# Kernel tuning notes

Hardware: AMD Instinct MI355X
Metric: run time of the kernel (lower is better)

The kernel has to match this reference:

```python
import jax, jax.numpy as jnp
import numpy as np

N_STATE = 1024
N_HEAD = 16
HEAD_DIM = N_STATE // N_HEAD


def setup_inputs() -> dict:
    key = jax.random.key(0)
    ks = jax.random.split(key, 8)
    s = 0.02
    return {
        "x": jax.random.normal(ks[0], (4, 1500, N_STATE), dtype=jnp.float32),
        "Wq": jax.random.normal(ks[1], (N_STATE, N_STATE), dtype=jnp.float32) * s,
        "bq": jnp.zeros((N_STATE,), dtype=jnp.float32),
        "Wk": jax.random.normal(ks[2], (N_STATE, N_STATE), dtype=jnp.float32) * s,
        "Wv": jax.random.normal(ks[3], (N_STATE, N_STATE), dtype=jnp.float32) * s,
        "bv": jnp.zeros((N_STATE,), dtype=jnp.float32),
        "Wo": jax.random.normal(ks[4], (N_STATE, N_STATE), dtype=jnp.float32) * s,
        "bo": jnp.zeros((N_STATE,), dtype=jnp.float32),
    }


def reference(x, Wq, bq, Wk, Wv, bv, Wo, bo):
    B, S, _ = x.shape
    scale = HEAD_DIM ** (-0.5)
    # projections (torch Linear: y = x @ W.T + b)
    q = x @ Wq.T + bq
    k = x @ Wk.T
    v = x @ Wv.T + bv
    # [B, H, S, D]
    q = q.reshape(B, S, N_HEAD, HEAD_DIM).transpose(0, 2, 1, 3)
    k = k.reshape(B, S, N_HEAD, HEAD_DIM).transpose(0, 2, 1, 3)
    v = v.reshape(B, S, N_HEAD, HEAD_DIM).transpose(0, 2, 1, 3)
    # scores scaled AFTER the matmul, as in the original (qk * qk_scale)
    qk = jnp.einsum("bhqd,bhkd->bhqk", q, k) * scale
    w = jax.nn.softmax(qk, axis=-1)
    wv = jnp.einsum("bhqk,bhkd->bhqd", w, v)
    wv = wv.transpose(0, 2, 1, 3).reshape(B, S, N_STATE)
    return wv @ Wo.T + bo
```

## Files before the change

kernel.cpp:

```cpp
#include <hip/hip_runtime.h>
#include <stdint.h>

#define S_LEN  1500
#define S_PAD  1536
#define BATCH  4
#define NSTATE 1024
#define NHEAD  16
#define HDIM   64
#define MROWS  6000
#define C1 0.180336879f

typedef __attribute__((ext_vector_type(8)))  short short8;
typedef __attribute__((ext_vector_type(4)))  float floatx4;
typedef __attribute__((ext_vector_type(16))) float floatx16;

__device__ __forceinline__ unsigned short f2bf(float f) {
  union { float f; unsigned int u; } v; v.f = f;
  unsigned int r = v.u + 0x7fffu + ((v.u >> 16) & 1u);
  return (unsigned short)(r >> 16);
}

__device__ __forceinline__ void gld_lds16(const void* g, void* l) {
  __builtin_amdgcn_global_load_lds(
      (const __attribute__((address_space(1))) void*)g,
      (__attribute__((address_space(3))) void*)l, 16, 0, 0);
}

__global__ __launch_bounds__(256) void cvt_all(
    const float* __restrict__ x,  const float* __restrict__ Wq,
    const float* __restrict__ Wk, const float* __restrict__ Wv,
    const float* __restrict__ Wo, unsigned short* __restrict__ dst)
{
  const size_t NX = (size_t)MROWS * NSTATE;
  size_t e = ((size_t)blockIdx.x * 256 + threadIdx.x) * 4;
  const float* src; size_t off;
  if (e < NX) { src = x; off = e; }
  else {
    size_t t = e - NX;
    int wsel = (int)(t >> 20);
    off = t & ((1u << 20) - 1);
    src = (wsel == 0) ? Wq : (wsel == 1) ? Wk : (wsel == 2) ? Wv : Wo;
  }
  float4 v = *(const float4*)(src + off);
  uint2 o;
  o.x = (unsigned int)f2bf(v.x) | ((unsigned int)f2bf(v.y) << 16);
  o.y = (unsigned int)f2bf(v.z) | ((unsigned int)f2bf(v.w) << 16);
  *(uint2*)(dst + e) = o;
}

template <bool F32OUT>
__device__ __forceinline__ void gemm128_bt(
    const unsigned short* __restrict__ X,
    const unsigned short* __restrict__ W,
    const float* __restrict__ bias,
    void* __restrict__ Yv,
    int m0, int n0, float oscale)
{
  __shared__ unsigned short As[2][128 * 32];
  __shared__ unsigned short Bs[2][128 * 32];

  const int tid  = threadIdx.x;
  const int lane = tid & 63;
  const int wid  = tid >> 6;
  const int wm   = (wid & 1) * 64;
  const int wn   = (wid >> 1) * 64;
  const int l15  = lane & 15;
  const int l4   = lane >> 4;

  floatx4 acc[4][4];
#pragma unroll
  for (int i = 0; i < 4; ++i)
#pragma unroll
    for (int j = 0; j < 4; ++j)
      acc[i][j] = (floatx4){0.f, 0.f, 0.f, 0.f};

  const int srow  = tid >> 2;
  const int scolb = (tid & 3) * 16;

  const char* xrp[2];
  const char* wrp[2];
#pragma unroll
  for (int r = 0; r < 2; ++r) {
    int arow = m0 + r * 64 + srow;
    if (arow > MROWS - 1) arow = MROWS - 1;
    xrp[r] = (const char*)X + (size_t)arow * NSTATE * 2 + scolb;
    int brow = n0 + r * 64 + srow;
    wrp[r] = (const char*)W + (size_t)brow * NSTATE * 2 + scolb;
  }

  for (int k0 = 0; k0 < NSTATE; k0 += 64) {
    __syncthreads();
#pragma unroll
    for (int h = 0; h < 2; ++h) {
      int kb = (k0 + h * 32) * 2;
#pragma unroll
      for (int r = 0; r < 2; ++r) {
        gld_lds16(xrp[r] + kb, (char*)As[h] + r * 4096 + wid * 1024);
        gld_lds16(wrp[r] + kb, (char*)Bs[h] + r * 4096 + wid * 1024);
      }
    }
    __syncthreads();

#pragma unroll
    for (int h = 0; h < 2; ++h) {
      short8 a[4], b[4];
#pragma unroll
      for (int i = 0; i < 4; ++i)
        a[i] = *(const short8*)(As[h] + (wm + i * 16 + l15) * 32 + l4 * 8);
#pragma unroll
      for (int j = 0; j < 4; ++j)
        b[j] = *(const short8*)(Bs[h] + (wn + j * 16 + l15) * 32 + l4 * 8);
#pragma unroll
      for (int i = 0; i < 4; ++i)
#pragma unroll
        for (int j = 0; j < 4; ++j)
          acc[i][j] = __builtin_amdgcn_mfma_f32_16x16x32_bf16(a[i], b[j], acc[i][j], 0, 0, 0);
    }
  }

#pragma unroll
  for (int j = 0; j < 4; ++j) {
    int ng = n0 + wn + j * 16 + l15;
    float bias_v = bias ? bias[ng] : 0.f;
#pragma unroll
    for (int i = 0; i < 4; ++i) {
      int mgb = m0 + wm + i * 16 + l4 * 4;
#pragma unroll
      for (int r = 0; r < 4; ++r) {
        int mg = mgb + r;
        if (mg < MROWS) {
          float val = (acc[i][j][r] + bias_v) * oscale;
          if (F32OUT) ((float*)Yv)[(size_t)mg * NSTATE + ng] = val;
          else        ((unsigned short*)Yv)[(size_t)mg * NSTATE + ng] = f2bf(val);
        }
      }
    }
  }
}

__global__ __launch_bounds__(256) void proj_qkv(
    const unsigned short* __restrict__ X,
    const unsigned short* __restrict__ Wq, const unsigned short* __restrict__ Wk,
    const unsigned short* __restrict__ Wv,
    const float* __restrict__ bq, const float* __restrict__ bv,
    unsigned short* __restrict__ q, unsigned short* __restrict__ k,
    unsigned short* __restrict__ v)
{
  const int id  = blockIdx.x;
  const int sid = (id & 7) * 141 + (id >> 3);
  const int z   = sid / 376;
  const int rem = sid - z * 376;
  const int m0  = (rem >> 3) * 128;
  const int n0  = (rem & 7) * 128;

  const unsigned short* W = (z == 0) ? Wq : (z == 1) ? Wk : Wv;
  const float* bias       = (z == 0) ? bq : (z == 1) ? (const float*)nullptr : bv;
  unsigned short* Y       = (z == 0) ? q  : (z == 1) ? k  : v;
  const float osc         = (z == 0) ? C1 : 1.0f;
  gemm128_bt<false>(X, W, bias, Y, m0, n0, osc);
}

__global__ __launch_bounds__(256) void proj_o(
    const unsigned short* __restrict__ X, const unsigned short* __restrict__ W,
    const float* __restrict__ bias, float* __restrict__ Y)
{
  const int id  = blockIdx.x;
  const int sid = (id & 7) * 47 + (id >> 3);
  gemm128_bt<true>(X, W, bias, Y, (sid >> 3) * 128, (sid & 7) * 128, 1.0f);
}

__global__ __launch_bounds__(256) void vtrans(
    const unsigned short* __restrict__ v, unsigned short* __restrict__ vt)
{
  __shared__ unsigned short T[64][72];
  const int tid = threadIdx.x;
  const int st = blockIdx.x * 64, h = blockIdx.y, b = blockIdx.z;
#pragma unroll
  for (int rr = 0; rr < 2; ++rr) {
    int sl = rr * 32 + (tid >> 3);
    int dl = (tid & 7) * 8;
    int s  = st + sl;
    uint4 val = make_uint4(0u, 0u, 0u, 0u);
    if (s < S_LEN)
      val = *(const uint4*)&v[((size_t)b * S_LEN + s) * NSTATE + h * HDIM + dl];
    *(uint4*)&T[sl][dl] = val;
  }
  __syncthreads();
#pragma unroll
  for (int rr = 0; rr < 2; ++rr) {
    int dl = rr * 32 + (tid >> 3);
    int s0 = (tid & 7) * 8;
    unsigned short tmp[8];
#pragma unroll
    for (int j2 = 0; j2 < 8; ++j2) tmp[j2] = T[s0 + j2][dl];
    *(uint4*)&vt[(((size_t)b * NHEAD + h) * HDIM + dl) * S_PAD + st + s0] =
        *(const uint4*)tmp;
  }
}

#define NHALF 24

__global__ __launch_bounds__(256, 4) void attn32t(
    const unsigned short* __restrict__ Q, const unsigned short* __restrict__ K,
    const unsigned short* __restrict__ VT, unsigned short* __restrict__ O)
{
  __shared__ unsigned short SMEM[16384];
  unsigned short* Os = SMEM;

  const int tid  = threadIdx.x;
  const int lane = tid & 63;
  const int w    = tid >> 6;
  const int l31  = lane & 31;
  const int lhi  = lane >> 5;

  const int id  = blockIdx.x;
  const int sid = (id & 7) * 96 + (id >> 3);
  const int qt  = sid % 12;
  const int hb  = sid / 12;
  const int h   = hb & 15;
  const int b   = hb >> 4;

  const size_t base  = ((size_t)b * S_LEN) * NSTATE + h * HDIM;
  const size_t vbase = (((size_t)b * NHEAD + h) * HDIM) * S_PAD;

  const int srow8 = lane >> 3;
  const int sc3   = lane & 7;

  short8 qf[4];
  {
    int qrow = qt * 128 + w * 32 + l31;
    if (qrow > S_LEN - 1) qrow = S_LEN - 1;
    const unsigned short* qp = Q + base + (size_t)qrow * NSTATE;
#pragma unroll
    for (int c = 0; c < 4; ++c)
      qf[c] = *(const short8*)(qp + c * 16 + lhi * 8);
  }

  short8 ones8;
#pragma unroll
  for (int i = 0; i < 8; ++i) ones8[i] = (short)0x3F80;

  floatx16 oacc[2];
  oacc[0] = (floatx16)(0.f);
  oacc[1] = (floatx16)(0.f);
  floatx16 lacc = (floatx16)(0.f);

  auto stage_half = [&](int u, int bi) {
    char* kbase = (char*)SMEM + bi * 8192;
    char* vbase_l = (char*)SMEM + 16384 + bi * 8192;
#pragma unroll
    for (int qq = 0; qq < 2; ++qq) {
      int cg   = w * 2 + qq;
      int row  = cg * 8 + srow8;
      int logc = sc3 ^ (row & 7);
      int s = u * 64 + row; if (s > S_LEN - 1) s = S_LEN - 1;
      gld_lds16(&K[base + (size_t)s * NSTATE + logc * 8], kbase + cg * 1024);
    }
#pragma unroll
    for (int qq = 0; qq < 2; ++qq) {
      int cg   = w * 2 + qq;
      int d    = cg * 8 + srow8;
      int logc = sc3 ^ (d & 7);
      gld_lds16(&VT[vbase + (size_t)d * S_PAD + u * 64 + logc * 8],
                vbase_l + cg * 1024);
    }
  };

  stage_half(0, 0);
  __syncthreads();

  for (int u = 0; u < NHALF; ++u) {
    const int cur = u & 1;
    if (u < NHALF - 1) stage_half(u + 1, cur ^ 1);

    const unsigned short* Ks  = SMEM + cur * 4096;
    const unsigned short* Vts = SMEM + 8192 + cur * 4096;

#pragma unroll
    for (int kvt = 0; kvt < 2; ++kvt) {
      int row = kvt * 32 + l31;
      floatx16 sacc = (floatx16)(0.f);
      __builtin_amdgcn_s_setprio(1);
#pragma unroll
      for (int c = 0; c < 4; ++c) {
        int phys = (c * 2 + lhi) ^ (row & 7);
        short8 ak = *(const short8*)(Ks + row * 64 + phys * 8);
        sacc = __builtin_amdgcn_mfma_f32_32x32x16_bf16(ak, qf[c], sacc, 0, 0, 0);
      }
      __builtin_amdgcn_s_setprio(0);

      if (u == NHALF - 1) {
        if (kvt == 1) {
#pragma unroll
          for (int r = 0; r < 16; ++r) sacc[r] = -3.0e38f;
        } else {
#pragma unroll
          for (int r = 12; r < 16; ++r) sacc[r] = lhi ? -3.0e38f : sacc[r];
        }
      }

      unsigned int pk[8], ex[8];
#pragma unroll
      for (int i = 0; i < 8; ++i) {
        float plo = exp2f(sacc[2 * i]);
        float phi = exp2f(sacc[2 * i + 1]);
        unsigned int rr;
        asm("v_cvt_pk_bf16_f32 %0, %1, %2" : "=v"(rr) : "v"(plo), "v"(phi));
        pk[i] = rr;
      }
#pragma unroll
      for (int i = 0; i < 8; ++i)
        ex[i] = __shfl_xor((unsigned int)pk[i], 32, 64);

      int4 f0i, f1i;
      f0i.x = lhi ? ex[2] : pk[0];
      f0i.y = lhi ? ex[3] : pk[1];
      f0i.z = lhi ? pk[2] : ex[0];
      f0i.w = lhi ? pk[3] : ex[1];
      f1i.x = lhi ? ex[6] : pk[4];
      f1i.y = lhi ? ex[7] : pk[5];
      f1i.z = lhi ? pk[6] : ex[4];
      f1i.w = lhi ? pk[7] : ex[5];
      short8 f0 = *(short8*)&f0i;
      short8 f1 = *(short8*)&f1i;

      __builtin_amdgcn_s_setprio(1);
      lacc = __builtin_amdgcn_mfma_f32_32x32x16_bf16(ones8, f0, lacc, 0, 0, 0);
      lacc = __builtin_amdgcn_mfma_f32_32x32x16_bf16(ones8, f1, lacc, 0, 0, 0);

#pragma unroll
      for (int dt = 0; dt < 2; ++dt) {
        int d = dt * 32 + l31;
        int p0 = ((kvt * 4 + 0) + lhi) ^ (d & 7);
        int p1 = ((kvt * 4 + 2) + lhi) ^ (d & 7);
        short8 av0 = *(const short8*)(Vts + d * 64 + p0 * 8);
        short8 av1 = *(const short8*)(Vts + d * 64 + p1 * 8);
        oacc[dt] = __builtin_amdgcn_mfma_f32_32x32x16_bf16(av0, f0, oacc[dt], 0, 0, 0);
        oacc[dt] = __builtin_amdgcn_mfma_f32_32x32x16_bf16(av1, f1, oacc[dt], 0, 0, 0);
      }
      __builtin_amdgcn_s_setprio(0);
    }

    __syncthreads();
  }

  float inv = 1.f / lacc[0];

  __syncthreads();
#pragma unroll
  for (int dt = 0; dt < 2; ++dt)
#pragma unroll
    for (int g = 0; g < 4; ++g) {
      int d0 = dt * 32 + g * 8 + lhi * 4;
      float v0 = oacc[dt][4 * g + 0] * inv;
      float v1 = oacc[dt][4 * g + 1] * inv;
      float v2 = oacc[dt][4 * g + 2] * inv;
      float v3 = oacc[dt][4 * g + 3] * inv;
      uint2 pk2;
      pk2.x = (unsigned int)f2bf(v0) | ((unsigned int)f2bf(v1) << 16);
      pk2.y = (unsigned int)f2bf(v2) | ((unsigned int)f2bf(v3) << 16);
      *(uint2*)&Os[(w * 32 + l31) * 72 + d0] = pk2;
    }
  __syncthreads();
#pragma unroll
  for (int pass = 0; pass < 4; ++pass) {
    int e = pass * 256 + tid;
    int row = e >> 3, ch = e & 7;
    int s = qt * 128 + row;
    if (s < S_LEN)
      *(uint4*)&O[base + (size_t)s * NSTATE + ch * 8] = *(const uint4*)&Os[row * 72 + ch * 8];
  }
}

extern "C" void kernel_launch(void* const* d_in, const int* in_sizes, int n_in,
                              void* d_out, int out_size, void* d_ws, size_t ws_size,
                              hipStream_t stream) {
  const float* x  = (const float*)d_in[0];
  const float* Wq = (const float*)d_in[1];
  const float* bq = (const float*)d_in[2];
  const float* Wk = (const float*)d_in[3];
  const float* Wv = (const float*)d_in[4];
  const float* bv = (const float*)d_in[5];
  const float* Wo = (const float*)d_in[6];
  const float* bo = (const float*)d_in[7];
  float* out = (float*)d_out;

  const size_t NX = (size_t)MROWS * NSTATE;
  const size_t NW = (size_t)NSTATE * NSTATE;

  unsigned short* xb  = (unsigned short*)d_ws;
  unsigned short* Wqb = xb  + NX;
  unsigned short* Wkb = Wqb + NW;
  unsigned short* Wvb = Wkb + NW;
  unsigned short* Wob = Wvb + NW;
  unsigned short* q   = Wob + NW;
  unsigned short* k   = q + NX;
  unsigned short* v   = k + NX;
  unsigned short* vt  = v + NX;
  unsigned short* wv  = xb;

  dim3 blk(256);
  const size_t n4_total = (NX + 4 * NW) / 4;
  cvt_all<<<dim3((int)(n4_total / 256)), blk, 0, stream>>>(x, Wq, Wk, Wv, Wo, xb);
  proj_qkv<<<dim3(1128), blk, 0, stream>>>(xb, Wqb, Wkb, Wvb, bq, bv, q, k, v);
  vtrans<<<dim3(24, NHEAD, BATCH), blk, 0, stream>>>(v, vt);
  attn32t<<<dim3(768), blk, 0, stream>>>(q, k, vt, wv);
  proj_o<<<dim3(376), blk, 0, stream>>>(wv, Wob, bo, out);
}
```

Measured before the change: 255.9 us.

## Switch projection GEMMs to 256x256 double-buffered swizzled LDS tiles

Replaces the 128x128 single-stage projection GEMM with a 256x256 tile computed by 512 threads (8 waves, each owning 128x64). The next K-slab is prefetched into a second LDS buffer while the current one is consumed, and the LDS layout is XOR-swizzled to avoid bank conflicts. Wave priority is raised around the MFMA burst. Each tile reuses more data and there is less barrier stalling. The cost is far fewer blocks (288 and 96) on a 256-CU device, about 128KB of LDS per block, and heavy register pressure, which can leave CUs idle and hurt the output projection in particular.

Result: slower. 300.0 us (+17.2%).

```diff
diff --git a/kernel.cpp b/kernel.cpp
--- a/kernel.cpp
+++ b/kernel.cpp
@@ -49,87 +49,106 @@
 }
 
 template <bool F32OUT>
-__device__ __forceinline__ void gemm128_bt(
+__device__ __forceinline__ void gemm256_db(
     const unsigned short* __restrict__ X,
     const unsigned short* __restrict__ W,
     const float* __restrict__ bias,
     void* __restrict__ Yv,
     int m0, int n0, float oscale)
 {
-  __shared__ unsigned short As[2][128 * 32];
-  __shared__ unsigned short Bs[2][128 * 32];
+  __shared__ unsigned short As[2][256 * 64];
+  __shared__ unsigned short Bs[2][256 * 64];
 
   const int tid  = threadIdx.x;
   const int lane = tid & 63;
-  const int wid  = tid >> 6;
-  const int wm   = (wid & 1) * 64;
-  const int wn   = (wid >> 1) * 64;
+  const int w    = tid >> 6;
+  const int wr   = (w >> 2) * 128;
+  const int wc   = (w & 3) * 64;
   const int l15  = lane & 15;
   const int l4   = lane >> 4;
-
-  floatx4 acc[4][4];
-#pragma unroll
-  for (int i = 0; i < 4; ++i)
-#pragma unroll
-    for (int j = 0; j < 4; ++j)
-      acc[i][j] = (floatx4){0.f, 0.f, 0.f, 0.f};
-
-  const int srow  = tid >> 2;
-  const int scolb = (tid & 3) * 16;
-
-  const char* xrp[2];
-  const char* wrp[2];
-#pragma unroll
-  for (int r = 0; r < 2; ++r) {
-    int arow = m0 + r * 64 + srow;
-    if (arow > MROWS - 1) arow = MROWS - 1;
-    xrp[r] = (const char*)X + (size_t)arow * NSTATE * 2 + scolb;
-    int brow = n0 + r * 64 + srow;
-    wrp[r] = (const char*)W + (size_t)brow * NSTATE * 2 + scolb;
-  }
-
-  for (int k0 = 0; k0 < NSTATE; k0 += 64) {
+  const int srow8 = lane >> 3;
+  const int sc    = lane & 7;
+
+  floatx4 acc[8][4];
+#pragma unroll
+  for (int m = 0; m < 8; ++m)
+#pragma unroll
+    for (int n = 0; n < 4; ++n)
+      acc[m][n] = (floatx4){0.f, 0.f, 0.f, 0.f};
+
+  const char* ap[4];
+  const char* bp[4];
+#pragma unroll
+  for (int c = 0; c < 4; ++c) {
+    int r    = c * 64 + w * 8 + srow8;
+    int logc = sc ^ srow8;
+    int gr = m0 + r; if (gr > MROWS - 1) gr = MROWS - 1;
+    ap[c] = (const char*)X + (size_t)gr * NSTATE * 2 + logc * 16;
+    int br = n0 + r;
+    bp[c] = (const char*)W + (size_t)br * NSTATE * 2 + logc * 16;
+  }
+
+  auto stage = [&](int t, int bi) {
+    const int kb = t * 128;
+#pragma unroll
+    for (int c = 0; c < 4; ++c) {
+      gld_lds16(ap[c] + kb, (char*)As[bi] + c * 8192 + w * 1024);
+      gld_lds16(bp[c] + kb, (char*)Bs[bi] + c * 8192 + w * 1024);
+    }
+  };
+
+  stage(0, 0);
+  __syncthreads();
+
+  for (int t = 0; t < 16; ++t) {
+    const int cur = t & 1;
+    if (t < 15) stage(t + 1, cur ^ 1);
+
+    const unsigned short* A = As[cur];
+    const unsigned short* B = Bs[cur];
+
+    short8 bfr[2][4];
+#pragma unroll
+    for (int s = 0; s < 2; ++s)
+#pragma unroll
+      for (int n = 0; n < 4; ++n) {
+        int r    = wc + n * 16 + l15;
+        int phys = (s * 4 + l4) ^ (r & 7);
+        bfr[s][n] = *(const short8*)(B + r * 64 + phys * 8);
+      }
+
+    __builtin_amdgcn_s_setprio(1);
+#pragma unroll
+    for (int m = 0; m < 8; ++m) {
+      int r  = wr + m * 16 + l15;
+      int p0 = (0 + l4) ^ (r & 7);
+      int p1 = (4 + l4) ^ (r & 7);
+      short8 a0 = *(const short8*)(A + r * 64 + p0 * 8);
+      short8 a1 = *(const short8*)(A + r * 64 + p1 * 8);
+#pragma unroll
+      for (int n = 0; n < 4; ++n)
+        acc[m][n] = __builtin_amdgcn_mfma_f32_16x16x32_bf16(a0, bfr[0][n], acc[m][n], 0, 0, 0);
+#pragma unroll
+      for (int n = 0; n < 4; ++n)
+        acc[m][n] = __builtin_amdgcn_mfma_f32_16x16x32_bf16(a1, bfr[1][n], acc[m][n], 0, 0, 0);
+    }
+    __builtin_amdgcn_s_setprio(0);
+
     __syncthreads();
-#pragma unroll
-    for (int h = 0; h < 2; ++h) {
-      int kb = (k0 + h * 32) * 2;
-#pragma unroll
-      for (int r = 0; r < 2; ++r) {
-        gld_lds16(xrp[r] + kb, (char*)As[h] + r * 4096 + wid * 1024);
-        gld_lds16(wrp[r] + kb, (char*)Bs[h] + r * 4096 + wid * 1024);
-      }
-    }
-    __syncthreads();
-
-#pragma unroll
-    for (int h = 0; h < 2; ++h) {
-      short8 a[4], b[4];
-#pragma unroll
-      for (int i = 0; i < 4; ++i)
-        a[i] = *(const short8*)(As[h] + (wm + i * 16 + l15) * 32 + l4 * 8);
-#pragma unroll
-      for (int j = 0; j < 4; ++j)
-        b[j] = *(const short8*)(Bs[h] + (wn + j * 16 + l15) * 32 + l4 * 8);
-#pragma unroll
-      for (int i = 0; i < 4; ++i)
-#pragma unroll
-        for (int j = 0; j < 4; ++j)
-          acc[i][j] = __builtin_amdgcn_mfma_f32_16x16x32_bf16(a[i], b[j], acc[i][j], 0, 0, 0);
-    }
-  }
-
-#pragma unroll
-  for (int j = 0; j < 4; ++j) {
-    int ng = n0 + wn + j * 16 + l15;
+  }
+
+#pragma unroll
+  for (int n = 0; n < 4; ++n) {
+    int ng = n0 + wc + n * 16 + l15;
     float bias_v = bias ? bias[ng] : 0.f;
 #pragma unroll
-    for (int i = 0; i < 4; ++i) {
-      int mgb = m0 + wm + i * 16 + l4 * 4;
-#pragma unroll
-      for (int r = 0; r < 4; ++r) {
-        int mg = mgb + r;
+    for (int m = 0; m < 8; ++m) {
+      int mgb = m0 + wr + m * 16 + l4 * 4;
+#pragma unroll
+      for (int ri = 0; ri < 4; ++ri) {
+        int mg = mgb + ri;
         if (mg < MROWS) {
-          float val = (acc[i][j][r] + bias_v) * oscale;
+          float val = (acc[m][n][ri] + bias_v) * oscale;
           if (F32OUT) ((float*)Yv)[(size_t)mg * NSTATE + ng] = val;
           else        ((unsigned short*)Yv)[(size_t)mg * NSTATE + ng] = f2bf(val);
         }
@@ -138,7 +157,7 @@
   }
 }
 
-__global__ __launch_bounds__(256) void proj_qkv(
+__global__ __launch_bounds__(512, 2) void proj_qkv(
     const unsigned short* __restrict__ X,
     const unsigned short* __restrict__ Wq, const unsigned short* __restrict__ Wk,
     const unsigned short* __restrict__ Wv,
@@ -147,26 +166,26 @@
     unsigned short* __restrict__ v)
 {
   const int id  = blockIdx.x;
-  const int sid = (id & 7) * 141 + (id >> 3);
-  const int z   = sid / 376;
-  const int rem = sid - z * 376;
-  const int m0  = (rem >> 3) * 128;
-  const int n0  = (rem & 7) * 128;
+  const int sid = (id & 7) * 36 + (id >> 3);
+  const int mt  = sid / 12;
+  const int rem = sid % 12;
+  const int z   = rem >> 2;
+  const int n0  = (rem & 3) * 256;
 
   const unsigned short* W = (z == 0) ? Wq : (z == 1) ? Wk : Wv;
   const float* bias       = (z == 0) ? bq : (z == 1) ? (const float*)nullptr : bv;
   unsigned short* Y       = (z == 0) ? q  : (z == 1) ? k  : v;
   const float osc         = (z == 0) ? C1 : 1.0f;
-  gemm128_bt<false>(X, W, bias, Y, m0, n0, osc);
-}
-
-__global__ __launch_bounds__(256) void proj_o(
+  gemm256_db<false>(X, W, bias, Y, mt * 256, n0, osc);
+}
+
+__global__ __launch_bounds__(512, 2) void proj_o(
     const unsigned short* __restrict__ X, const unsigned short* __restrict__ W,
     const float* __restrict__ bias, float* __restrict__ Y)
 {
   const int id  = blockIdx.x;
-  const int sid = (id & 7) * 47 + (id >> 3);
-  gemm128_bt<true>(X, W, bias, Y, (sid >> 3) * 128, (sid & 7) * 128, 1.0f);
+  const int sid = (id & 7) * 12 + (id >> 3);
+  gemm256_db<true>(X, W, bias, Y, (sid >> 2) * 256, (sid & 3) * 256, 1.0f);
 }
 
 __global__ __launch_bounds__(256) void vtrans(
@@ -399,11 +418,10 @@
   unsigned short* vt  = v + NX;
   unsigned short* wv  = xb;
 
-  dim3 blk(256);
   const size_t n4_total = (NX + 4 * NW) / 4;
-  cvt_all<<<dim3((int)(n4_total / 256)), blk, 0, stream>>>(x, Wq, Wk, Wv, Wo, xb);
-  proj_qkv<<<dim3(1128), blk, 0, stream>>>(xb, Wqb, Wkb, Wvb, bq, bv, q, k, v);
-  vtrans<<<dim3(24, NHEAD, BATCH), blk, 0, stream>>>(v, vt);
-  attn32t<<<dim3(768), blk, 0, stream>>>(q, k, vt, wv);
-  proj_o<<<dim3(376), blk, 0, stream>>>(wv, Wob, bo, out);
-}
+  cvt_all<<<dim3((int)(n4_total / 256)), dim3(256), 0, stream>>>(x, Wq, Wk, Wv, Wo, xb);
+  proj_qkv<<<dim3(288), dim3(512), 0, stream>>>(xb, Wqb, Wkb, Wvb, bq, bv, q, k, v);
+  vtrans<<<dim3(24, NHEAD, BATCH), dim3(256), 0, stream>>>(v, vt);
+  attn32t<<<dim3(768), dim3(256), 0, stream>>>(q, k, vt, wv);
+  proj_o<<<dim3(96), dim3(512), 0, stream>>>(wv, Wob, bo, out);
+}
```

## Switch GEMMs to 32x32 MFMA with swizzled LDS and fuse V transpose into projection

Applied to the files above, without the earlier changes.

The shared GEMM now uses 32x32x16 bf16 MFMA tiles with an XOR-swizzled LDS layout in place of 16x16x32 tiles, aiming to cut LDS bank conflicts and instruction count. The V projection epilogue writes straight into the transposed, padded vt layout, which removes the separate vtrans kernel and the round trip through an intermediate v buffer. A memset zeroes the padding of vt on each call. The transposed epilogue issues scattered 8-byte stores with a per-element division to recover the batch index, which may hurt store coalescing.

Result: no change. 256.1 us (+0.1%).

```diff
diff --git a/kernel.cpp b/kernel.cpp
--- a/kernel.cpp
+++ b/kernel.cpp
@@ -48,13 +48,12 @@
   *(uint2*)(dst + e) = o;
 }
 
-template <bool F32OUT>
-__device__ __forceinline__ void gemm128_bt(
+__device__ __forceinline__ void gemm128_32(
     const unsigned short* __restrict__ X,
     const unsigned short* __restrict__ W,
     const float* __restrict__ bias,
     void* __restrict__ Yv,
-    int m0, int n0, float oscale)
+    int m0, int n0, float oscale, int outmode)
 {
   __shared__ unsigned short As[2][128 * 32];
   __shared__ unsigned short Bs[2][128 * 32];
@@ -64,18 +63,19 @@
   const int wid  = tid >> 6;
   const int wm   = (wid & 1) * 64;
   const int wn   = (wid >> 1) * 64;
-  const int l15  = lane & 15;
-  const int l4   = lane >> 4;
-
-  floatx4 acc[4][4];
-#pragma unroll
-  for (int i = 0; i < 4; ++i)
-#pragma unroll
-    for (int j = 0; j < 4; ++j)
-      acc[i][j] = (floatx4){0.f, 0.f, 0.f, 0.f};
-
-  const int srow  = tid >> 2;
-  const int scolb = (tid & 3) * 16;
+  const int l31  = lane & 31;
+  const int lhi  = lane >> 5;
+  const int fr   = (l31 >> 1) & 3;
+
+  floatx16 acc[2][2];
+#pragma unroll
+  for (int i = 0; i < 2; ++i)
+#pragma unroll
+    for (int j = 0; j < 2; ++j)
+      acc[i][j] = (floatx16)(0.f);
+
+  const int srow = tid >> 2;
+  const int logc = (lane & 3) ^ ((srow >> 1) & 3);
 
   const char* xrp[2];
   const char* wrp[2];
@@ -83,9 +83,9 @@
   for (int r = 0; r < 2; ++r) {
     int arow = m0 + r * 64 + srow;
     if (arow > MROWS - 1) arow = MROWS - 1;
-    xrp[r] = (const char*)X + (size_t)arow * NSTATE * 2 + scolb;
+    xrp[r] = (const char*)X + (size_t)arow * NSTATE * 2 + logc * 16;
     int brow = n0 + r * 64 + srow;
-    wrp[r] = (const char*)W + (size_t)brow * NSTATE * 2 + scolb;
+    wrp[r] = (const char*)W + (size_t)brow * NSTATE * 2 + logc * 16;
   }
 
   for (int k0 = 0; k0 < NSTATE; k0 += 64) {
@@ -103,37 +103,77 @@
 
 #pragma unroll
     for (int h = 0; h < 2; ++h) {
-      short8 a[4], b[4];
-#pragma unroll
-      for (int i = 0; i < 4; ++i)
-        a[i] = *(const short8*)(As[h] + (wm + i * 16 + l15) * 32 + l4 * 8);
-#pragma unroll
-      for (int j = 0; j < 4; ++j)
-        b[j] = *(const short8*)(Bs[h] + (wn + j * 16 + l15) * 32 + l4 * 8);
-#pragma unroll
-      for (int i = 0; i < 4; ++i)
-#pragma unroll
-        for (int j = 0; j < 4; ++j)
-          acc[i][j] = __builtin_amdgcn_mfma_f32_16x16x32_bf16(a[i], b[j], acc[i][j], 0, 0, 0);
-    }
-  }
-
-#pragma unroll
-  for (int j = 0; j < 4; ++j) {
-    int ng = n0 + wn + j * 16 + l15;
-    float bias_v = bias ? bias[ng] : 0.f;
-#pragma unroll
-    for (int i = 0; i < 4; ++i) {
-      int mgb = m0 + wm + i * 16 + l4 * 4;
-#pragma unroll
-      for (int r = 0; r < 4; ++r) {
-        int mg = mgb + r;
-        if (mg < MROWS) {
-          float val = (acc[i][j][r] + bias_v) * oscale;
-          if (F32OUT) ((float*)Yv)[(size_t)mg * NSTATE + ng] = val;
-          else        ((unsigned short*)Yv)[(size_t)mg * NSTATE + ng] = f2bf(val);
+      short8 af[2][2], bf[2][2];
+#pragma unroll
+      for (int mt = 0; mt < 2; ++mt)
+#pragma unroll
+        for (int kc = 0; kc < 2; ++kc) {
+          int row  = wm + mt * 32 + l31;
+          int phys = (kc * 2 + lhi) ^ fr;
+          af[mt][kc] = *(const short8*)(As[h] + row * 32 + phys * 8);
         }
-      }
+#pragma unroll
+      for (int nt = 0; nt < 2; ++nt)
+#pragma unroll
+        for (int kc = 0; kc < 2; ++kc) {
+          int row  = wn + nt * 32 + l31;
+          int phys = (kc * 2 + lhi) ^ fr;
+          bf[nt][kc] = *(const short8*)(Bs[h] + row * 32 + phys * 8);
+        }
+#pragma unroll
+      for (int mt = 0; mt < 2; ++mt)
+#pragma unroll
+        for (int nt = 0; nt < 2; ++nt)
+#pragma unroll
+          for (int kc = 0; kc < 2; ++kc)
+            acc[mt][nt] = __builtin_amdgcn_mfma_f32_32x32x16_bf16(
+                af[mt][kc], bf[nt][kc], acc[mt][nt], 0, 0, 0);
+    }
+  }
+
+  if (outmode == 2) {
+    unsigned short* vt = (unsigned short*)Yv;
+#pragma unroll
+    for (int nt = 0; nt < 2; ++nt) {
+      int ng = n0 + wn + nt * 32 + l31;
+      float bias_v = bias[ng];
+      int d  = ng & 63;
+      int hh = ng >> 6;
+#pragma unroll
+      for (int mt = 0; mt < 2; ++mt)
+#pragma unroll
+        for (int rq = 0; rq < 4; ++rq) {
+          int mgq = m0 + wm + mt * 32 + 8 * rq + 4 * lhi;
+          if (mgq < MROWS) {
+            int bb = mgq / 1500;
+            int s0 = mgq - 1500 * bb;
+            float v0 = acc[mt][nt][rq * 4 + 0] + bias_v;
+            float v1 = acc[mt][nt][rq * 4 + 1] + bias_v;
+            float v2 = acc[mt][nt][rq * 4 + 2] + bias_v;
+            float v3 = acc[mt][nt][rq * 4 + 3] + bias_v;
+            uint2 pk2;
+            pk2.x = (unsigned int)f2bf(v0) | ((unsigned int)f2bf(v1) << 16);
+            pk2.y = (unsigned int)f2bf(v2) | ((unsigned int)f2bf(v3) << 16);
+            *(uint2*)&vt[(((size_t)bb * NHEAD + hh) * HDIM + d) * S_PAD + s0] = pk2;
+          }
+        }
+    }
+  } else {
+#pragma unroll
+    for (int nt = 0; nt < 2; ++nt) {
+      int ng = n0 + wn + nt * 32 + l31;
+      float bias_v = bias ? bias[ng] : 0.f;
+#pragma unroll
+      for (int mt = 0; mt < 2; ++mt)
+#pragma unroll
+        for (int r = 0; r < 16; ++r) {
+          int mg = m0 + wm + mt * 32 + (r & 3) + 8 * (r >> 2) + 4 * lhi;
+          if (mg < MROWS) {
+            float val = (acc[mt][nt][r] + bias_v) * oscale;
+            if (outmode == 1) ((float*)Yv)[(size_t)mg * NSTATE + ng] = val;
+            else ((unsigned short*)Yv)[(size_t)mg * NSTATE + ng] = f2bf(val);
+          }
+        }
     }
   }
 }
@@ -144,7 +184,7 @@
     const unsigned short* __restrict__ Wv,
     const float* __restrict__ bq, const float* __restrict__ bv,
     unsigned short* __restrict__ q, unsigned short* __restrict__ k,
-    unsigned short* __restrict__ v)
+    unsigned short* __restrict__ vt)
 {
   const int id  = blockIdx.x;
   const int sid = (id & 7) * 141 + (id >> 3);
@@ -153,11 +193,9 @@
   const int m0  = (rem >> 3) * 128;
   const int n0  = (rem & 7) * 128;
 
-  const unsigned short* W = (z == 0) ? Wq : (z == 1) ? Wk : Wv;
-  const float* bias       = (z == 0) ? bq : (z == 1) ? (const float*)nullptr : bv;
-  unsigned short* Y       = (z == 0) ? q  : (z == 1) ? k  : v;
-  const float osc         = (z == 0) ? C1 : 1.0f;
-  gemm128_bt<false>(X, W, bias, Y, m0, n0, osc);
+  if (z == 0)      gemm128_32(X, Wq, bq, q,  m0, n0, C1,  0);
+  else if (z == 1) gemm128_32(X, Wk, (const float*)nullptr, k, m0, n0, 1.0f, 0);
+  else             gemm128_32(X, Wv, bv, vt, m0, n0, 1.0f, 2);
 }
 
 __global__ __launch_bounds__(256) void proj_o(
@@ -166,36 +204,7 @@
 {
   const int id  = blockIdx.x;
   const int sid = (id & 7) * 47 + (id >> 3);
-  gemm128_bt<true>(X, W, bias, Y, (sid >> 3) * 128, (sid & 7) * 128, 1.0f);
-}
-
-__global__ __launch_bounds__(256) void vtrans(
-    const unsigned short* __restrict__ v, unsigned short* __restrict__ vt)
-{
-  __shared__ unsigned short T[64][72];
-  const int tid = threadIdx.x;
-  const int st = blockIdx.x * 64, h = blockIdx.y, b = blockIdx.z;
-#pragma unroll
-  for (int rr = 0; rr < 2; ++rr) {
-    int sl = rr * 32 + (tid >> 3);
-    int dl = (tid & 7) * 8;
-    int s  = st + sl;
-    uint4 val = make_uint4(0u, 0u, 0u, 0u);
-    if (s < S_LEN)
-      val = *(const uint4*)&v[((size_t)b * S_LEN + s) * NSTATE + h * HDIM + dl];
-    *(uint4*)&T[sl][dl] = val;
-  }
-  __syncthreads();
-#pragma unroll
-  for (int rr = 0; rr < 2; ++rr) {
-    int dl = rr * 32 + (tid >> 3);
-    int s0 = (tid & 7) * 8;
-    unsigned short tmp[8];
-#pragma unroll
-    for (int j2 = 0; j2 < 8; ++j2) tmp[j2] = T[s0 + j2][dl];
-    *(uint4*)&vt[(((size_t)b * NHEAD + h) * HDIM + dl) * S_PAD + st + s0] =
-        *(const uint4*)tmp;
-  }
+  gemm128_32(X, W, bias, Y, (sid >> 3) * 128, (sid & 7) * 128, 1.0f, 1);
 }
 
 #define NHALF 24
@@ -385,8 +394,9 @@
   const float* bo = (const float*)d_in[7];
   float* out = (float*)d_out;
 
-  const size_t NX = (size_t)MROWS * NSTATE;
-  const size_t NW = (size_t)NSTATE * NSTATE;
+  const size_t NX  = (size_t)MROWS * NSTATE;
+  const size_t NW  = (size_t)NSTATE * NSTATE;
+  const size_t NVT = (size_t)BATCH * NHEAD * HDIM * S_PAD;
 
   unsigned short* xb  = (unsigned short*)d_ws;
   unsigned short* Wqb = xb  + NX;
@@ -395,15 +405,14 @@
   unsigned short* Wob = Wvb + NW;
   unsigned short* q   = Wob + NW;
   unsigned short* k   = q + NX;
-  unsigned short* v   = k + NX;
-  unsigned short* vt  = v + NX;
+  unsigned short* vt  = k + NX;
   unsigned short* wv  = xb;
 
-  dim3 blk(256);
+  hipMemsetAsync(vt, 0, NVT * 2, stream);
+
   const size_t n4_total = (NX + 4 * NW) / 4;
-  cvt_all<<<dim3((int)(n4_total / 256)), blk, 0, stream>>>(x, Wq, Wk, Wv, Wo, xb);
-  proj_qkv<<<dim3(1128), blk, 0, stream>>>(xb, Wqb, Wkb, Wvb, bq, bv, q, k, v);
-  vtrans<<<dim3(24, NHEAD, BATCH), blk, 0, stream>>>(v, vt);
-  attn32t<<<dim3(768), blk, 0, stream>>>(q, k, vt, wv);
-  proj_o<<<dim3(376), blk, 0, stream>>>(wv, Wob, bo, out);
-}
+  cvt_all<<<dim3((int)(n4_total / 256)), dim3(256), 0, stream>>>(x, Wq, Wk, Wv, Wo, xb);
+  proj_qkv<<<dim3(1128), dim3(256), 0, stream>>>(xb, Wqb, Wkb, Wvb, bq, bv, q, k, vt);
+  attn32t<<<dim3(768), dim3(256), 0, stream>>>(q, k, vt, wv);
+  proj_o<<<dim3(376), dim3(256), 0, stream>>>(wv, Wob, bo, out);
+}
```
